# Performance work log

Hardware: AMD Instinct MI355X
Metric: run time of the kernel (lower is better)

The kernel has to match this reference:

```python
import jax, jax.numpy as jnp
import numpy as np

B, S, D_IN, D_OUT = 8, 2048, 512, 512


def setup_inputs() -> dict:
    key = jax.random.key(0)
    ks = jax.random.split(key, 6)
    return {
        "inputs_for_keys": jax.random.normal(ks[0], (B, S, D_IN), dtype=jnp.float32),
        "inputs_for_values": jax.random.normal(ks[1], (B, S, D_IN), dtype=jnp.float32),
        "inputs_for_queries": jax.random.normal(ks[2], (B, S, D_IN), dtype=jnp.float32),
        "Wq": jax.random.normal(ks[3], (D_IN, D_OUT), dtype=jnp.float32) * 0.05,
        "Wk": jax.random.normal(ks[4], (D_IN, D_OUT), dtype=jnp.float32) * 0.05,
        "Wv": jax.random.normal(ks[5], (D_IN, D_OUT), dtype=jnp.float32) * 0.05,
    }


def reference(inputs_for_keys, inputs_for_values, inputs_for_queries, Wq, Wk, Wv):
    # Projections: [B,S,D_in] @ [D_in,D_out] -> [B,S,D_out]
    Q = inputs_for_queries @ Wq
    K = inputs_for_keys @ Wk
    V = inputs_for_values @ Wv
    d_k = K.shape[-1]
    scale = 1.0 / jnp.sqrt(jnp.float32(d_k))
    # Scores: [B,Sq,Sk]
    scores = jnp.einsum("bqd,bkd->bqk", Q, K) * scale
    # Causal mask: original adds -inf for key positions j > query i (use_mask=True)
    q_idx = jnp.arange(Q.shape[1])[:, None]
    k_idx = jnp.arange(K.shape[1])[None, :]
    scores = jnp.where(k_idx > q_idx, jnp.float32(-jnp.inf), scores)
    attn = jax.nn.softmax(scores, axis=-1)
    return jnp.einsum("bqk,bkd->bqd", attn, V)
```

## Files before the change

kernel.cpp:

```cpp
#include <hip/hip_runtime.h>
#include <hip/hip_bf16.h>

typedef __bf16 bf16;
typedef __bf16 bf16x4 __attribute__((ext_vector_type(4)));
typedef __bf16 bf16x8 __attribute__((ext_vector_type(8)));
typedef float f32x4 __attribute__((ext_vector_type(4)));
typedef float f32x16 __attribute__((ext_vector_type(16)));

#define NB 8
#define NS 2048
#define ND 512

static __device__ __forceinline__ f32x4 mfma16(bf16x8 a, bf16x8 b, f32x4 c) {
  return __builtin_amdgcn_mfma_f32_16x16x32_bf16(a, b, c, 0, 0, 0);
}
static __device__ __forceinline__ f32x16 mfma32(bf16x8 a, bf16x8 b, f32x16 c) {
  return __builtin_amdgcn_mfma_f32_32x32x16_bf16(a, b, c, 0, 0, 0);
}
static __device__ __forceinline__ void async16(const bf16* g, bf16* l) {
  __builtin_amdgcn_global_load_lds((const __attribute__((address_space(1))) void*)g,
                                   (__attribute__((address_space(3))) void*)l, 16, 0, 0);
}

#define WAVE_VM0() asm volatile("s_waitcnt vmcnt(0)" ::: "memory")
#define BLK_BAR() do { asm volatile("s_waitcnt lgkmcnt(0)" ::: "memory"); \
  __builtin_amdgcn_s_barrier(); __builtin_amdgcn_sched_barrier(0); } while (0)

__global__ void wconv_kernel(const float* __restrict__ Wq,
                             const float* __restrict__ Wk,
                             const float* __restrict__ Wv,
                             bf16* __restrict__ Wt) {
  __shared__ float buf[64][65];
  const int z = blockIdx.z;
  const float* W = (z == 0) ? Wq : (z == 1) ? Wk : Wv;
  const float scale = (z == 0) ? 0.063763537f : 1.0f;
  const int k0 = blockIdx.x * 64, n0 = blockIdx.y * 64;
  const int t = threadIdx.x;
#pragma unroll
  for (int i = 0; i < 16; ++i) {
    int idx = i * 256 + t;
    int kk = idx >> 6, nn = idx & 63;
    buf[kk][nn] = W[(size_t)(k0 + kk) * 512 + n0 + nn];
  }
  __syncthreads();
#pragma unroll
  for (int i = 0; i < 16; ++i) {
    int idx = i * 256 + t;
    int nn = idx >> 6, kk = idx & 63;
    Wt[(size_t)z * 262144 + (size_t)(n0 + nn) * 512 + k0 + (kk ^ ((nn & 7) << 3))] =
        (bf16)(buf[kk][nn] * scale);
  }
}

__launch_bounds__(256)
__global__ void proj_kernel(const float* __restrict__ Xq,
                            const float* __restrict__ Xk,
                            const float* __restrict__ Xv,
                            const bf16* __restrict__ Wt,
                            bf16* __restrict__ Cq,
                            bf16* __restrict__ Ck,
                            bf16* __restrict__ Cv) {
  __shared__ bf16 As[2][128][72];
  __shared__ bf16 WsL[2][8192];
  const int z = blockIdx.z;
  const float* A = (z == 0) ? Xq : (z == 1) ? Xk : Xv;
  const bf16* Wz = Wt + (size_t)z * 262144;
  bf16* C = (z == 0) ? Cq : (z == 1) ? Ck : Cv;

  const int t = threadIdx.x;
  const int lane = t & 63;
  const int w = t >> 6;
  const int wr = w >> 1, wc = w & 1;
  const int bxr = blockIdx.x;
  const int mt = (bxr & 7) * 16 + (bxr >> 3);
  const int bm = mt * 128;
  const int bn = blockIdx.y * 128;

  f32x4 acc[4][4] = {};

  auto stageA = [&](int kc, int bufi) {
    int r0 = t >> 4, seg = t & 15;
#pragma unroll
    for (int p = 0; p < 8; ++p) {
      int r = p * 16 + r0;
      float4 v = *(const float4*)(A + (size_t)(bm + r) * 512 + kc * 64 + seg * 4);
      bf16x4 o = {(bf16)v.x, (bf16)v.y, (bf16)v.z, (bf16)v.w};
      *(bf16x4*)&As[bufi][r][seg * 4] = o;
    }
  };
  auto stageW = [&](int kc, int bufi) {
    const int n = t >> 3, seg = t & 7;
#pragma unroll
    for (int i = 0; i < 4; ++i)
      async16(Wz + (size_t)(bn + i * 32 + n) * 512 + kc * 64 + seg * 8,
              &WsL[bufi][(i * 32 + n) * 64 + seg * 8]);
  };

  stageW(0, 0);
  stageA(0, 0);
  __syncthreads();
  int buf = 0;
  for (int kc = 0; kc < 8; ++kc) {
    if (kc < 7) { stageW(kc + 1, buf ^ 1); stageA(kc + 1, buf ^ 1); }
    const int arow = lane & 15, kq = (lane >> 4) * 8;
#pragma unroll
    for (int kk = 0; kk < 2; ++kk) {
      bf16x8 af[4], bfr[4];
#pragma unroll
      for (int mi = 0; mi < 4; ++mi)
        af[mi] = *(const bf16x8*)&As[buf][wr * 64 + mi * 16 + arow][kk * 32 + kq];
#pragma unroll
      for (int ni = 0; ni < 4; ++ni) {
        int n = wc * 64 + ni * 16 + arow;
        bfr[ni] = *(const bf16x8*)&WsL[buf][n * 64 + ((kk * 32 + kq) ^ ((n & 7) << 3))];
      }
#pragma unroll
      for (int mi = 0; mi < 4; ++mi)
#pragma unroll
        for (int ni = 0; ni < 4; ++ni)
          acc[mi][ni] = mfma16(af[mi], bfr[ni], acc[mi][ni]);
    }
    __syncthreads();
    buf ^= 1;
  }

  const int row0 = (lane >> 4) * 4, col = lane & 15;
#pragma unroll
  for (int mi = 0; mi < 4; ++mi)
#pragma unroll
    for (int ni = 0; ni < 4; ++ni) {
      int cg = bn + wc * 64 + ni * 16 + col;
#pragma unroll
      for (int j = 0; j < 4; ++j) {
        int rg = bm + wr * 64 + mi * 16 + row0 + j;
        bf16 o = (bf16)acc[mi][ni][j];
        if (z == 0) {
          C[(size_t)rg * ND + cg] = o;
        } else if (z == 1) {
          C[(size_t)rg * ND + (cg ^ ((rg & 7) << 3))] = o;
        } else {
          int bb = rg >> 11, s = rg & 2047;
          int ss = (s & ~63) | ((s & 63) ^ ((cg & 7) << 3));
          C[(size_t)bb * (ND * NS) + (size_t)cg * NS + ss] = o;
        }
      }
    }
}

__launch_bounds__(512, 2)
__global__ void attn_kernel(const bf16* __restrict__ Qg,
                            const bf16* __restrict__ Kg,
                            const bf16* __restrict__ Vtg,
                            bf16* __restrict__ Pn,
                            float* __restrict__ Mp,
                            float* __restrict__ Lp) {
  __shared__ bf16 Ks[64][512];
  __shared__ bf16 Vts[512][64];
  __shared__ bf16 Sx[64][68];
  __shared__ bf16 Ps[2][64][76];
  __shared__ float r_lds[2][64];
  __shared__ float l_lds[64];

  const int t = threadIdx.x;
  const int lane = t & 63;
  const int w = t >> 6;
  const int l31 = lane & 31, lhi = lane >> 5;
  const int wq = w & 3;
  const bool isQK = w < 4;
  const int qh = wq & 1, skh = wq >> 1;
  const int dofs = wq * 128;

  const int id = blockIdx.x;
  const int b = id & 7;
  const int qt = 31 - ((id >> 3) & 31);
  const int h = id >> 8;
  const int q0 = qt * 64;
  const int nt = qt + 1, mid = (nt + 1) >> 1;
  const int t_begin = h ? mid : 0;
  const int t_end = h ? nt : mid;
  const int NT = t_end - t_begin;
  const int pidx = (h * 8 + b) * 32 + qt;

  const bf16* Qb = Qg + (size_t)b * NS * ND;
  const bf16* Kb = Kg + (size_t)b * NS * ND;
  const bf16* Vb = Vtg + (size_t)b * ND * NS;

  if (isQK) {
    const int ql = qh * 32 + l31;
    const int qg = q0 + ql;
    bf16x8 qf[16];
    float m_run = -1e30f, l_run = 0.0f;
    if (NT > 0) {
      const bf16* qrow = Qb + (size_t)qg * ND + skh * 256 + lhi * 8;
#pragma unroll
      for (int kc = 0; kc < 16; ++kc) qf[kc] = *(const bf16x8*)(qrow + kc * 16);
#pragma unroll
      for (int i = 0; i < 16; ++i)
        async16(Kb + (size_t)(t_begin * 64 + wq * 16 + i) * ND + lane * 8,
                &Ks[wq * 16 + i][0]);
    }
    for (int s = 0; s <= NT; ++s) {
      const int it = t_begin + s;
      f32x16 s0 = {}, s1 = {};
      if (s < NT) WAVE_VM0();
      BLK_BAR();
      if (s < NT) {
        __builtin_amdgcn_s_setprio(1);
#pragma unroll
        for (int kc = 0; kc < 16; ++kc) {
          const int colk = (skh * 256 + kc * 16 + lhi * 8) ^ ((l31 & 7) << 3);
          bf16x8 kf0 = *(const bf16x8*)&Ks[l31][colk];
          bf16x8 kf1 = *(const bf16x8*)&Ks[32 + l31][colk];
          s0 = mfma32(kf0, qf[kc], s0);
          s1 = mfma32(kf1, qf[kc], s1);
        }
        __builtin_amdgcn_s_setprio(0);
        if (skh) {
#pragma unroll
          for (int jg = 0; jg < 4; ++jg) {
            bf16x4 a = {(bf16)s0[jg * 4 + 0], (bf16)s0[jg * 4 + 1],
                        (bf16)s0[jg * 4 + 2], (bf16)s0[jg * 4 + 3]};
            bf16x4 c = {(bf16)s1[jg * 4 + 0], (bf16)s1[jg * 4 + 1],
                        (bf16)s1[jg * 4 + 2], (bf16)s1[jg * 4 + 3]};
            *(bf16x4*)&Sx[ql][jg * 8 + 4 * lhi] = a;
            *(bf16x4*)&Sx[ql][32 + jg * 8 + 4 * lhi] = c;
          }
        }
      }
      BLK_BAR();
      if (s < NT) {
        if (it + 1 < t_end) {
#pragma unroll
          for (int i = 0; i < 16; ++i)
            async16(Kb + (size_t)((it + 1) * 64 + wq * 16 + i) * ND + lane * 8,
                    &Ks[wq * 16 + i][0]);
        }
        if (!skh) {
          float v[32];
#pragma unroll
          for (int jg = 0; jg < 4; ++jg) {
            bf16x4 a = *(const bf16x4*)&Sx[ql][jg * 8 + 4 * lhi];
            bf16x4 c = *(const bf16x4*)&Sx[ql][32 + jg * 8 + 4 * lhi];
#pragma unroll
            for (int e = 0; e < 4; ++e) {
              v[jg * 4 + e] = s0[jg * 4 + e] + (float)a[e];
              v[16 + jg * 4 + e] = s1[jg * 4 + e] + (float)c[e];
            }
          }
          if (it == qt) {
            const int k0 = it * 64;
#pragma unroll
            for (int j = 0; j < 16; ++j) {
              int kv = k0 + (j & 3) + 8 * (j >> 2) + 4 * lhi;
              if (kv > qg) v[j] = -1e30f;
              if (kv + 32 > qg) v[16 + j] = -1e30f;
            }
          }
          float mx = v[0];
#pragma unroll
          for (int j = 1; j < 32; ++j) mx = fmaxf(mx, v[j]);
          mx = fmaxf(mx, __shfl_xor(mx, 32));
          float mn = fmaxf(m_run, mx);
          float rr = exp2f(m_run - mn);
          float sum = 0.0f;
#pragma unroll
          for (int j = 0; j < 32; ++j) { v[j] = exp2f(v[j] - mn); sum += v[j]; }
          sum += __shfl_xor(sum, 32);
          m_run = mn;
          l_run = l_run * rr + sum;
          if (lhi == 0) r_lds[it & 1][ql] = rr;
#pragma unroll
          for (int jg = 0; jg < 4; ++jg) {
            bf16x4 a = {(bf16)v[jg * 4 + 0], (bf16)v[jg * 4 + 1],
                        (bf16)v[jg * 4 + 2], (bf16)v[jg * 4 + 3]};
            bf16x4 c = {(bf16)v[16 + jg * 4 + 0], (bf16)v[16 + jg * 4 + 1],
                        (bf16)v[16 + jg * 4 + 2], (bf16)v[16 + jg * 4 + 3]};
            *(bf16x4*)&Ps[it & 1][ql][jg * 8 + 4 * lhi] = a;
            *(bf16x4*)&Ps[it & 1][ql][32 + jg * 8 + 4 * lhi] = c;
          }
        }
      }
    }
    if (!skh && lhi == 0) {
      Mp[pidx * 64 + ql] = m_run;
      Lp[pidx * 64 + ql] = l_run;
      l_lds[ql] = l_run;
    }
    BLK_BAR();
  } else {
    f32x16 acc[2][4] = {};
    if (NT > 0) {
#pragma unroll
      for (int i = 0; i < 16; ++i) {
        int d = dofs + i * 8 + (lane >> 3);
        async16(Vb + (size_t)d * NS + t_begin * 64 + (lane & 7) * 8,
                &Vts[dofs + i * 8][0]);
      }
    }
    for (int s = 0; s <= NT; ++s) {
      const int it = t_begin + s;
      if (s >= 1) WAVE_VM0();
      BLK_BAR();
      bf16x8 paf[2][4];
      if (s >= 1) {
        const int bb = (it - 1) & 1;
#pragma unroll
        for (int qb = 0; qb < 2; ++qb)
#pragma unroll
          for (int j = 0; j < 16; ++j) {
            float rr = r_lds[bb][qb * 32 + (j & 3) + 8 * (j >> 2) + 4 * lhi];
#pragma unroll
            for (int dt = 0; dt < 4; ++dt) acc[qb][dt][j] *= rr;
          }
#pragma unroll
        for (int qb = 0; qb < 2; ++qb)
#pragma unroll
          for (int kc = 0; kc < 4; ++kc)
            paf[qb][kc] = *(const bf16x8*)&Ps[bb][qb * 32 + l31][kc * 16 + lhi * 8];
        __builtin_amdgcn_s_setprio(1);
#pragma unroll
        for (int dt = 0; dt < 2; ++dt) {
          const int d = dofs + dt * 32 + l31;
          const int swzv = (d & 7) << 3;
#pragma unroll
          for (int kc = 0; kc < 4; ++kc) {
            bf16x8 vf = *(const bf16x8*)&Vts[d][(kc * 16 + lhi * 8) ^ swzv];
            acc[0][dt] = mfma32(paf[0][kc], vf, acc[0][dt]);
            acc[1][dt] = mfma32(paf[1][kc], vf, acc[1][dt]);
          }
        }
        __builtin_amdgcn_s_setprio(0);
      }
      BLK_BAR();
      if (s >= 1) {
        __builtin_amdgcn_s_setprio(1);
#pragma unroll
        for (int dt = 2; dt < 4; ++dt) {
          const int d = dofs + dt * 32 + l31;
          const int swzv = (d & 7) << 3;
#pragma unroll
          for (int kc = 0; kc < 4; ++kc) {
            bf16x8 vf = *(const bf16x8*)&Vts[d][(kc * 16 + lhi * 8) ^ swzv];
            acc[0][dt] = mfma32(paf[0][kc], vf, acc[0][dt]);
            acc[1][dt] = mfma32(paf[1][kc], vf, acc[1][dt]);
          }
        }
        __builtin_amdgcn_s_setprio(0);
        asm volatile("s_waitcnt lgkmcnt(0)" ::: "memory");
        if (it < t_end) {
#pragma unroll
          for (int i = 0; i < 16; ++i) {
            int d = dofs + i * 8 + (lane >> 3);
            async16(Vb + (size_t)d * NS + it * 64 + (lane & 7) * 8,
                    &Vts[dofs + i * 8][0]);
          }
        }
      }
    }
    BLK_BAR();
    bf16* Ob = Pn + (size_t)pidx * 64 * ND;
#pragma unroll
    for (int qb = 0; qb < 2; ++qb)
#pragma unroll
      for (int j = 0; j < 16; ++j) {
        const int row = qb * 32 + (j & 3) + 8 * (j >> 2) + 4 * lhi;
        float lv = l_lds[row];
        float linv = (lv > 0.0f) ? 1.0f / lv : 0.0f;
#pragma unroll
        for (int dt = 0; dt < 4; ++dt)
          Ob[(size_t)row * ND + dofs + dt * 32 + l31] = (bf16)(acc[qb][dt][j] * linv);
      }
  }
}

__global__ void combine_kernel(const bf16* __restrict__ Pn,
                               const float* __restrict__ Mp,
                               const float* __restrict__ Lp,
                               float* __restrict__ Out) {
  const int total = NB * NS * ND / 4;
  for (int v = blockIdx.x * 256 + threadIdx.x; v < total; v += gridDim.x * 256) {
    int e = v * 4;
    int d = e & 511;
    int s = (e >> 9) & 2047;
    int bb = e >> 20;
    int qt = s >> 6, r = s & 63;
    int p0 = (bb * 32 + qt) * 64 + r;
    int p1 = ((8 + bb) * 32 + qt) * 64 + r;
    float m0 = Mp[p0], l0 = Lp[p0], m1 = Mp[p1], l1 = Lp[p1];
    float M = fmaxf(m0, m1);
    float w0 = l0 * exp2f(m0 - M), w1 = l1 * exp2f(m1 - M);
    float inv = 1.0f / (w0 + w1);
    bf16x4 o0 = *(const bf16x4*)(Pn + (size_t)p0 * ND + d);
    bf16x4 o1 = *(const bf16x4*)(Pn + (size_t)p1 * ND + d);
    f32x4 o;
    o[0] = (w0 * (float)o0[0] + w1 * (float)o1[0]) * inv;
    o[1] = (w0 * (float)o0[1] + w1 * (float)o1[1]) * inv;
    o[2] = (w0 * (float)o0[2] + w1 * (float)o1[2]) * inv;
    o[3] = (w0 * (float)o0[3] + w1 * (float)o1[3]) * inv;
    __builtin_nontemporal_store(o, (f32x4*)(Out + e));
  }
}

extern "C" void kernel_launch(void* const* d_in, const int* in_sizes, int n_in,
                              void* d_out, int out_size, void* d_ws, size_t ws_size,
                              hipStream_t stream) {
  const float* Xk = (const float*)d_in[0];
  const float* Xv = (const float*)d_in[1];
  const float* Xq = (const float*)d_in[2];
  const float* Wq = (const float*)d_in[3];
  const float* Wk = (const float*)d_in[4];
  const float* Wv = (const float*)d_in[5];
  float* Out = (float*)d_out;

  char* ws = (char*)d_ws;
  bf16* Qb = (bf16*)(ws);
  bf16* Kb = (bf16*)(ws + (size_t)16 * 1024 * 1024);
  bf16* Vt = (bf16*)(ws + (size_t)32 * 1024 * 1024);
  bf16* Wt = (bf16*)(ws + (size_t)48 * 1024 * 1024);
  bf16* Pn = (bf16*)(ws + (size_t)50 * 1024 * 1024);
  float* Mp = (float*)(ws + (size_t)82 * 1024 * 1024);
  float* Lp = (float*)(ws + (size_t)82 * 1024 * 1024 + 131072);

  wconv_kernel<<<dim3(8, 8, 3), 256, 0, stream>>>(Wq, Wk, Wv, Wt);
  proj_kernel<<<dim3(128, 4, 3), 256, 0, stream>>>(Xq, Xk, Xv, Wt, Qb, Kb, Vt);
  attn_kernel<<<512, 512, 0, stream>>>(Qb, Kb, Vt, Pn, Mp, Lp);
  combine_kernel<<<2048, 256, 0, stream>>>(Pn, Mp, Lp, Out);
}
```

Baseline: 152.1 us.

## Software-pipeline projection GEMM A loads through registers with manual vmcnt waits

The projection GEMM used to load each fp32 A tile and write it to LDS in the same step. It now splits this into a register-staged global load issued two k-chunks ahead and a later bf16 conversion and LDS write. The W async-to-LDS copies are issued at the top of each iteration. Explicit s_waitcnt vmcnt/lgkmcnt counts plus raw s_barrier replace __syncthreads, so global memory latency overlaps the MFMA work. This costs extra registers (8 float4) and relies on hand-counted outstanding-load numbers being correct.

Measured after the change: 146.8 us (median of 2 runs). 1.04x faster.

```diff
diff --git a/kernel.cpp b/kernel.cpp
--- a/kernel.cpp
+++ b/kernel.cpp
@@ -75,44 +75,55 @@
   const int mt = (bxr & 7) * 16 + (bxr >> 3);
   const int bm = mt * 128;
   const int bn = blockIdx.y * 128;
+  const int r0 = t >> 4, seg = t & 15;
 
   f32x4 acc[4][4] = {};
-
-  auto stageA = [&](int kc, int bufi) {
-    int r0 = t >> 4, seg = t & 15;
+  float4 ar[8];
+
+  auto loadA = [&](int kc) {
+#pragma unroll
+    for (int p = 0; p < 8; ++p)
+      ar[p] = *(const float4*)(A + (size_t)(bm + p * 16 + r0) * 512 + kc * 64 + seg * 4);
+  };
+  auto writeA = [&](int bufi) {
 #pragma unroll
     for (int p = 0; p < 8; ++p) {
-      int r = p * 16 + r0;
-      float4 v = *(const float4*)(A + (size_t)(bm + r) * 512 + kc * 64 + seg * 4);
-      bf16x4 o = {(bf16)v.x, (bf16)v.y, (bf16)v.z, (bf16)v.w};
-      *(bf16x4*)&As[bufi][r][seg * 4] = o;
+      bf16x4 o = {(bf16)ar[p].x, (bf16)ar[p].y, (bf16)ar[p].z, (bf16)ar[p].w};
+      *(bf16x4*)&As[bufi][p * 16 + r0][seg * 4] = o;
     }
   };
-  auto stageW = [&](int kc, int bufi) {
-    const int n = t >> 3, seg = t & 7;
+  auto issueW = [&](int kc, int bufi) {
+    const int n = t >> 3, sg8 = t & 7;
 #pragma unroll
     for (int i = 0; i < 4; ++i)
-      async16(Wz + (size_t)(bn + i * 32 + n) * 512 + kc * 64 + seg * 8,
-              &WsL[bufi][(i * 32 + n) * 64 + seg * 8]);
+      async16(Wz + (size_t)(bn + i * 32 + n) * 512 + kc * 64 + sg8 * 8,
+              &WsL[bufi][(i * 32 + n) * 64 + sg8 * 8]);
   };
 
-  stageW(0, 0);
-  stageA(0, 0);
-  __syncthreads();
-  int buf = 0;
+  loadA(0);
+  WAVE_VM0();
+  writeA(0);
+  issueW(0, 0);
+  loadA(1);
+  asm volatile("s_waitcnt vmcnt(8) lgkmcnt(0)" ::: "memory");
+  __builtin_amdgcn_s_barrier();
+  __builtin_amdgcn_sched_barrier(0);
+
+#pragma unroll
   for (int kc = 0; kc < 8; ++kc) {
-    if (kc < 7) { stageW(kc + 1, buf ^ 1); stageA(kc + 1, buf ^ 1); }
+    const int c = kc & 1;
+    if (kc < 7) issueW(kc + 1, c ^ 1);
     const int arow = lane & 15, kq = (lane >> 4) * 8;
 #pragma unroll
     for (int kk = 0; kk < 2; ++kk) {
       bf16x8 af[4], bfr[4];
 #pragma unroll
       for (int mi = 0; mi < 4; ++mi)
-        af[mi] = *(const bf16x8*)&As[buf][wr * 64 + mi * 16 + arow][kk * 32 + kq];
+        af[mi] = *(const bf16x8*)&As[c][wr * 64 + mi * 16 + arow][kk * 32 + kq];
 #pragma unroll
       for (int ni = 0; ni < 4; ++ni) {
         int n = wc * 64 + ni * 16 + arow;
-        bfr[ni] = *(const bf16x8*)&WsL[buf][n * 64 + ((kk * 32 + kq) ^ ((n & 7) << 3))];
+        bfr[ni] = *(const bf16x8*)&WsL[c][n * 64 + ((kk * 32 + kq) ^ ((n & 7) << 3))];
       }
 #pragma unroll
       for (int mi = 0; mi < 4; ++mi)
@@ -120,8 +131,18 @@
         for (int ni = 0; ni < 4; ++ni)
           acc[mi][ni] = mfma16(af[mi], bfr[ni], acc[mi][ni]);
     }
-    __syncthreads();
-    buf ^= 1;
+    if (kc < 7) {
+      asm volatile("s_waitcnt vmcnt(4)" ::: "memory");
+      writeA(c ^ 1);
+      if (kc < 6) {
+        loadA(kc + 2);
+        asm volatile("s_waitcnt vmcnt(8) lgkmcnt(0)" ::: "memory");
+      } else {
+        asm volatile("s_waitcnt vmcnt(0) lgkmcnt(0)" ::: "memory");
+      }
+      __builtin_amdgcn_s_barrier();
+      __builtin_amdgcn_sched_barrier(0);
+    }
   }
 
   const int row0 = (lane >> 4) * 4, col = lane & 15;
```
